# Kernel optimization log

Hardware: AMD Instinct MI355X
Metric: run time of the kernel (lower is better)

Reference implementation:

```python
import jax, jax.numpy as jnp
import numpy as np

B, T, C, H = 2, 2048, 1024, 16
D = C // H  # head dim = 64


def setup_inputs() -> dict:
    key = jax.random.key(0)
    ks = jax.random.split(key, 3)
    x = jax.random.normal(ks[0], (B, T, C), dtype=jnp.float32)
    W_attn = jax.random.normal(ks[1], (C, 3 * C), dtype=jnp.float32) * (1.0 / np.sqrt(C))
    b_attn = jnp.zeros((3 * C,), dtype=jnp.float32)
    W_proj = jax.random.normal(ks[2], (C, C), dtype=jnp.float32) * (1.0 / np.sqrt(C))
    b_proj = jnp.zeros((C,), dtype=jnp.float32)
    return {"x": x, "W_attn": W_attn, "b_attn": b_attn, "W_proj": W_proj, "b_proj": b_proj}


def reference(x, W_attn, b_attn, W_proj, b_proj):
    Bb, Tt, Cc = x.shape
    qkv = x @ W_attn + b_attn                       # [B,T,3C]
    q, k, v = jnp.split(qkv, 3, axis=-1)            # each [B,T,C]
    q = q.reshape(Bb, Tt, H, D).transpose(0, 2, 1, 3)  # [B,H,T,D]
    k = k.reshape(Bb, Tt, H, D).transpose(0, 2, 1, 3)
    v = v.reshape(Bb, Tt, H, D).transpose(0, 2, 1, 3)
    # NOTE: original scales by 1/sqrt(n_embd), not 1/sqrt(head_dim)
    scale = 1.0 / np.sqrt(Cc)
    wei = jnp.einsum('bhqd,bhkd->bhqk', q, k) * scale  # [B,H,T,T]
    causal = jnp.tril(jnp.ones((Tt, Tt), dtype=bool))
    wei = jnp.where(causal, wei, -jnp.inf)
    wei = jax.nn.softmax(wei, axis=-1)
    out = jnp.einsum('bhqk,bhkd->bhqd', wei, v)        # [B,H,T,D]
    out = out.transpose(0, 2, 1, 3).reshape(Bb, Tt, Cc)
    return out @ W_proj + b_proj
```

## Files before the change

### kernel.cpp

```cpp
#include <hip/hip_runtime.h>


typedef short bfrag __attribute__((ext_vector_type(8)));
typedef float facc  __attribute__((ext_vector_type(4)));
typedef float f16v  __attribute__((ext_vector_type(16)));
typedef float f4v   __attribute__((ext_vector_type(4)));
typedef unsigned int u32x2 __attribute__((ext_vector_type(2)));
typedef unsigned int u32x4v __attribute__((ext_vector_type(4)));
typedef unsigned short u16;

#define MFMA16(a, b, c) __builtin_amdgcn_mfma_f32_16x16x32_bf16((a), (b), (c), 0, 0, 0)
#define MFMA32(a, b, c) __builtin_amdgcn_mfma_f32_32x32x16_bf16((a), (b), (c), 0, 0, 0)

__device__ __forceinline__ u16 f2bf(float f) {
  union { float f; unsigned u; } v; v.f = f;
  unsigned r = v.u + 0x7fffu + ((v.u >> 16) & 1u);
  return (u16)(r >> 16);
}

__device__ __forceinline__ unsigned cvtpk(float lo, float hi) {
  unsigned r;
  asm("v_cvt_pk_bf16_f32 %0, %1, %2" : "=v"(r) : "v"(lo), "v"(hi));
  return r;
}

__device__ __forceinline__ void async_lds16(const void* g, void* l) {
  __builtin_amdgcn_global_load_lds(
      (const __attribute__((address_space(1))) unsigned char*)g,
      (__attribute__((address_space(3))) unsigned char*)l, 16, 0, 0);
}


__global__ void cast_bf16_kernel(const float* __restrict__ s, u16* __restrict__ d, int n) {
  int i = (blockIdx.x * blockDim.x + threadIdx.x) * 4;
  if (i >= n) return;
  f4v v = *reinterpret_cast<const f4v*>(s + i);
  u32x2 w;
  w[0] = (unsigned)f2bf(v[0]) | ((unsigned)f2bf(v[1]) << 16);
  w[1] = (unsigned)f2bf(v[2]) | ((unsigned)f2bf(v[3]) << 16);
  *reinterpret_cast<u32x2*>(d + i) = w;
}

__global__ void transpose_cast_kernel(const float* __restrict__ src, u16* __restrict__ dst,
                                      int K, int N) {
  __shared__ float tile[32][33];
  int tx = threadIdx.x, ty = threadIdx.y;
  int n0 = blockIdx.x * 32, k0 = blockIdx.y * 32;
  for (int j = ty; j < 32; j += 8)
    tile[j][tx] = src[(size_t)(k0 + j) * N + (n0 + tx)];
  __syncthreads();
  for (int j = ty; j < 32; j += 8)
    dst[(size_t)(n0 + j) * K + (k0 + tx)] = f2bf(tile[tx][j]);
}


template <int EPI>
__global__ __launch_bounds__(256) void gemm_kernel(
    const u16* __restrict__ A, const u16* __restrict__ Bt,
    const float* __restrict__ bias, float* __restrict__ outf,
    u16* __restrict__ qb, u16* __restrict__ kb, u16* __restrict__ vb) {
  constexpr int KD = 1024;
  __shared__ u16 As[128 * 32];
  __shared__ u16 Bs[128 * 32];
  const int t = threadIdx.x;
  const int l = t & 63, w = t >> 6;
  const int wm = w >> 1, wn = w & 1;
  const int lg = l >> 4, lc = l & 15;
  const int m0 = blockIdx.y * 128, n0 = blockIdx.x * 128;
  facc acc[4][4] = {};
  const int srow = t >> 2, scol = (t & 3) * 8;
  const u16* ga = A + (size_t)(m0 + srow) * KD + scol;
  const u16* gb = Bt + (size_t)(n0 + srow) * KD + scol;
  u16* la0 = As + t * 8;  u16* la1 = As + 2048 + t * 8;
  u16* lb0 = Bs + t * 8;  u16* lb1 = Bs + 2048 + t * 8;
  for (int kt = 0; kt < KD / 32; ++kt) {
    __syncthreads();
    async_lds16(ga + kt * 32, la0);
    async_lds16(ga + 64 * KD + kt * 32, la1);
    async_lds16(gb + kt * 32, lb0);
    async_lds16(gb + 64 * KD + kt * 32, lb1);
    __syncthreads();
    bfrag a[4], b[4];
#pragma unroll
    for (int mi = 0; mi < 4; ++mi)
      a[mi] = *reinterpret_cast<const bfrag*>(As + (wm * 64 + mi * 16 + lc) * 32 + lg * 8);
#pragma unroll
    for (int ni = 0; ni < 4; ++ni)
      b[ni] = *reinterpret_cast<const bfrag*>(Bs + (wn * 64 + ni * 16 + lc) * 32 + lg * 8);
#pragma unroll
    for (int mi = 0; mi < 4; ++mi)
#pragma unroll
      for (int ni = 0; ni < 4; ++ni)
        acc[mi][ni] = MFMA16(a[mi], b[ni], acc[mi][ni]);
  }
#pragma unroll
  for (int mi = 0; mi < 4; ++mi) {
#pragma unroll
    for (int ni = 0; ni < 4; ++ni) {
#pragma unroll
      for (int r = 0; r < 4; ++r) {
        int gm = m0 + wm * 64 + mi * 16 + lg * 4 + r;
        int gn = n0 + wn * 64 + ni * 16 + lc;
        float val = acc[mi][ni][r] + bias[gn];
        if constexpr (EPI == 0) {
          int sec = gn >> 10, ci = gn & 1023;
          int h = ci >> 6, d = ci & 63;
          int b_ = gm >> 11, tq = gm & 2047;
          int bh = b_ * 16 + h;
          if (sec == 0) {
            qb[((size_t)bh * 2048 + tq) * 64 + d] = f2bf(val * 0.045084439f);
          } else if (sec == 1) {
            kb[((size_t)bh * 2048 + tq) * 64 + d] = f2bf(val);
          } else {
            vb[((size_t)bh * 64 + d) * 2048 + tq] = f2bf(val);
          }
        } else {
          outf[(size_t)gm * 1024 + gn] = val;
        }
      }
    }
  }
}


__global__ __launch_bounds__(128, 2) void attn_kernel(
    const u16* __restrict__ Qb, const u16* __restrict__ Kb,
    const u16* __restrict__ Vtb, u16* __restrict__ attn) {
  constexpr int T = 2048;
  __shared__ u16 Ks[2][2][64 * 64];
  const int t = threadIdx.x;
  const int l = t & 63, w = t >> 6;
  const int c = l & 31, h = l >> 5;
  const int b = blockIdx.x;
  const int bh = b & 31;
  const int chunk = 63 - (b >> 5);
  const int ntile = (chunk >> 1) + 1;
  const int nrounds = (ntile + 1) >> 1;
  const int q0 = chunk * 32;
  const size_t base = (size_t)bh * T * 64;
  const u16* Qp = Qb + base;
  const u16* Kp = Kb + base;
  const u16* Vp = Vtb + base;

  bfrag qf[4];
#pragma unroll
  for (int dt = 0; dt < 4; ++dt)
    qf[dt] = *reinterpret_cast<const bfrag*>(Qp + (size_t)(q0 + c) * 64 + dt * 16 + 8 * h);

  f16v o[2] = {};
  f16v s[2];
  float m_ = -1e30f, l_ = 0.f;

  const int srow0 = l >> 3;
  const int sw8   = ((l & 7) ^ (l >> 3)) * 8;
  u16* kb0 = &Ks[0][w][0];
  u16* kb1 = &Ks[1][w][0];

#define STAGE_K(dst, kvb_)                                                       \
  {                                                                              \
    _Pragma("unroll")                                                            \
    for (int j = 0; j < 8; ++j)                                                  \
      async_lds16(Kp + (size_t)((kvb_) + srow0 + 8 * j) * 64 + sw8,              \
                  (dst) + 512 * j);                                              \
  }
#define LOADV(vf, kvb_)                                                          \
  {                                                                              \
    _Pragma("unroll")                                                            \
    for (int nt = 0; nt < 2; ++nt)                                               \
      _Pragma("unroll")                                                          \
      for (int k2 = 0; k2 < 4; ++k2)                                             \
        vf[nt * 4 + k2] = *reinterpret_cast<const bfrag*>(                       \
            Vp + (size_t)(32 * nt + c) * T + (kvb_) + 16 * k2 + 8 * h);          \
  }

  auto qk = [&](const u16* ks) {
    const f16v z = {};
    s[0] = z; s[1] = z;
    __builtin_amdgcn_s_setprio(1);
#pragma unroll
    for (int kt = 0; kt < 2; ++kt)
#pragma unroll
      for (int dt = 0; dt < 4; ++dt) {
        const bfrag a = *reinterpret_cast<const bfrag*>(
            ks + (32 * kt + c) * 64 + (((2 * dt + h) ^ (c & 7)) * 8));
        s[kt] = MFMA32(a, qf[dt], s[kt]);
      }
    __builtin_amdgcn_s_setprio(0);
  };

  auto pv = [&](const bfrag pa[4], const bfrag vf[8]) {
    __builtin_amdgcn_s_setprio(1);
#pragma unroll
    for (int nt = 0; nt < 2; ++nt)
#pragma unroll
      for (int k2 = 0; k2 < 4; ++k2)
        o[nt] = MFMA32(pa[k2], vf[nt * 4 + k2], o[nt]);
    __builtin_amdgcn_s_setprio(0);
  };

  auto softmax_pa = [&](int it, bfrag pa[4]) {
    if (it == ntile - 1) {
      const int kvb = 64 * it;
      const int qq = q0 + c;
#pragma unroll
      for (int kt = 0; kt < 2; ++kt)
#pragma unroll
        for (int r = 0; r < 16; ++r) {
          const int kk = kvb + 32 * kt + (r & 3) + 8 * (r >> 2) + 4 * h;
          if (kk > qq) s[kt][r] = -1e30f;
        }
    }
    float pms[4] = {-1e30f, -1e30f, -1e30f, -1e30f};
#pragma unroll
    for (int kt = 0; kt < 2; ++kt)
#pragma unroll
      for (int r = 0; r < 16; ++r) pms[r & 3] = fmaxf(pms[r & 3], s[kt][r]);
    float pm = fmaxf(fmaxf(pms[0], pms[1]), fmaxf(pms[2], pms[3]));
    pm = fmaxf(pm, __shfl_xor(pm, 32));
    if (!__all(pm <= m_ + 8.0f)) {
      const float mn = fmaxf(m_, pm);
      const float al = exp2f(m_ - mn);
      l_ *= al;
#pragma unroll
      for (int r = 0; r < 16; ++r) {
        const float ar = __shfl(al, (r & 3) + 8 * (r >> 2) + 4 * h);
        o[0][r] *= ar;
        o[1][r] *= ar;
      }
      m_ = mn;
    }
    float ps[4] = {0.f, 0.f, 0.f, 0.f};
#pragma unroll
    for (int kt = 0; kt < 2; ++kt)
#pragma unroll
      for (int r = 0; r < 16; ++r) {
        const float e = exp2f(s[kt][r] - m_);
        s[kt][r] = e;
        ps[r & 3] += e;
      }
    float pss = (ps[0] + ps[1]) + (ps[2] + ps[3]);
    pss += __shfl_xor(pss, 32);
    l_ += pss;
#pragma unroll
    for (int kt = 0; kt < 2; ++kt)
#pragma unroll
      for (int sub = 0; sub < 2; ++sub) {
        const int bs = 8 * sub;
        unsigned x1 = cvtpk(s[kt][bs + 0], s[kt][bs + 1]);
        unsigned y1 = cvtpk(s[kt][bs + 4], s[kt][bs + 5]);
        asm volatile("v_permlane32_swap_b32 %0, %1" : "+v"(x1), "+v"(y1));
        unsigned x2 = cvtpk(s[kt][bs + 2], s[kt][bs + 3]);
        unsigned y2 = cvtpk(s[kt][bs + 6], s[kt][bs + 7]);
        asm volatile("v_permlane32_swap_b32 %0, %1" : "+v"(x2), "+v"(y2));
        union { u32x4v wv; bfrag f; } u;
        u.wv[0] = x1; u.wv[1] = x2; u.wv[2] = y1; u.wv[3] = y2;
        pa[2 * kt + sub] = u.f;
      }
  };

  bfrag vfA[8], vfB[8], pa[4];
  if (w < ntile) { STAGE_K(kb0, 64 * w); LOADV(vfA, 64 * w); }
  __syncthreads();
  for (int r = 0; r < nrounds; ++r) {
    const int it = 2 * r + w;
    const int itn = it + 2;
    if (itn < ntile) {
      if (r & 1) { STAGE_K(kb0, 64 * itn); LOADV(vfA, 64 * itn); }
      else       { STAGE_K(kb1, 64 * itn); LOADV(vfB, 64 * itn); }
    }
    if (it < ntile) {
      qk((r & 1) ? kb1 : kb0);
      softmax_pa(it, pa);
      pv(pa, (r & 1) ? vfB : vfA);
    }
    __syncthreads();
  }

  float* Fo = (float*)&Ks[0][0][0];
  float* Fm = Fo + 64 * 33;
  float* Fl = Fm + 32;
  if (w == 1) {
#pragma unroll
    for (int nt = 0; nt < 2; ++nt)
#pragma unroll
      for (int r = 0; r < 16; ++r) {
        const int row = (r & 3) + 8 * (r >> 2) + 4 * h;
        Fo[(nt * 32 + c) * 33 + row] = o[nt][r];
      }
    if (h == 0) { Fm[c] = m_; Fl[c] = l_; }
  }
  __syncthreads();
  if (w == 0) {
    const float m1v = Fm[c], l1v = Fl[c];
    const float mm = fmaxf(m_, m1v);
    const float a0 = exp2f(m_ - mm), a1 = exp2f(m1v - mm);
    const float linv = 1.0f / (a0 * l_ + a1 * l1v);
    const int b_ = bh >> 4, hd = bh & 15;
#pragma unroll
    for (int r = 0; r < 16; ++r) {
      const int row = (r & 3) + 8 * (r >> 2) + 4 * h;
      const float a0r = __shfl(a0, row);
      const float a1r = __shfl(a1, row);
      const float lr = __shfl(linv, row);
      const int tq = q0 + row;
#pragma unroll
      for (int nt = 0; nt < 2; ++nt) {
        const float o1 = Fo[(nt * 32 + c) * 33 + row];
        attn[((size_t)(b_ * T + tq)) * 1024 + hd * 64 + 32 * nt + c] =
            f2bf((a0r * o[nt][r] + a1r * o1) * lr);
      }
    }
  }
#undef STAGE_K
#undef LOADV
}


extern "C" void kernel_launch(void* const* d_in, const int* in_sizes, int n_in,
                              void* d_out, int out_size, void* d_ws, size_t ws_size,
                              hipStream_t stream) {
  const float* x      = (const float*)d_in[0];
  const float* W_attn = (const float*)d_in[1];
  const float* b_attn = (const float*)d_in[2];
  const float* W_proj = (const float*)d_in[3];
  const float* b_proj = (const float*)d_in[4];
  float* out = (float*)d_out;
  char* ws = (char*)d_ws;
  u16* xb   = (u16*)(ws);
  u16* Wat  = (u16*)(ws + (8u  << 20));
  u16* Wpt  = (u16*)(ws + (14u << 20));
  u16* Qb   = (u16*)(ws + (16u << 20));
  u16* Kb   = (u16*)(ws + (24u << 20));
  u16* Vtb  = (u16*)(ws + (32u << 20));
  u16* attn = (u16*)(ws + (40u << 20));

  cast_bf16_kernel<<<4096, 256, 0, stream>>>(x, xb, 4096 * 1024);
  transpose_cast_kernel<<<dim3(96, 32), dim3(32, 8), 0, stream>>>(W_attn, Wat, 1024, 3072);
  transpose_cast_kernel<<<dim3(32, 32), dim3(32, 8), 0, stream>>>(W_proj, Wpt, 1024, 1024);
  gemm_kernel<0><<<dim3(24, 32), 256, 0, stream>>>(xb, Wat, b_attn, nullptr, Qb, Kb, Vtb);
  attn_kernel<<<2048, 128, 0, stream>>>(Qb, Kb, Vtb, attn);
  gemm_kernel<1><<<dim3(8, 32), 256, 0, stream>>>(attn, Wpt, b_proj, out, nullptr, nullptr, nullptr);
}
```

Measured before the change: 138.8 us.

## Double-buffer GEMM LDS, swizzle GEMM blocks, share K tiles across attention query warps

The GEMM now double-buffers its A/B LDS tiles so the next k-slice loads while the current one computes. It also drops from two barriers to one per k-step and remaps block indices with an 8-way swizzle to improve L2 locality. The attention kernel goes from 128 to 256 threads, so two query sub-blocks of 32 rows share each staged 64-row K tile in LDS, halving K staging per query row and halving the grid. The costs are more LDS per GEMM block and a larger attention block with different occupancy, and the swizzle assumes the grid size is divisible by 8.

```diff
diff --git a/kernel.cpp b/kernel.cpp
--- a/kernel.cpp
+++ b/kernel.cpp
@@ -58,41 +58,51 @@
 __global__ __launch_bounds__(256) void gemm_kernel(
     const u16* __restrict__ A, const u16* __restrict__ Bt,
     const float* __restrict__ bias, float* __restrict__ outf,
-    u16* __restrict__ qb, u16* __restrict__ kb, u16* __restrict__ vb) {
-  constexpr int KD = 1024;
-  __shared__ u16 As[128 * 32];
-  __shared__ u16 Bs[128 * 32];
+    u16* __restrict__ qb, u16* __restrict__ kb, u16* __restrict__ vb, int NX) {
+  constexpr int KD = 1024, NK = KD / 32;
+  __shared__ u16 As[2][128 * 32];
+  __shared__ u16 Bs[2][128 * 32];
   const int t = threadIdx.x;
   const int l = t & 63, w = t >> 6;
   const int wm = w >> 1, wn = w & 1;
   const int lg = l >> 4, lc = l & 15;
-  const int m0 = blockIdx.y * 128, n0 = blockIdx.x * 128;
+  const int nwg = gridDim.x;
+  const int u = blockIdx.x;
+  const int swz = (u & 7) * (nwg >> 3) + (u >> 3);
+  const int m0 = (swz / NX) * 128, n0 = (swz % NX) * 128;
   facc acc[4][4] = {};
   const int srow = t >> 2, scol = (t & 3) * 8;
   const u16* ga = A + (size_t)(m0 + srow) * KD + scol;
   const u16* gb = Bt + (size_t)(n0 + srow) * KD + scol;
-  u16* la0 = As + t * 8;  u16* la1 = As + 2048 + t * 8;
-  u16* lb0 = Bs + t * 8;  u16* lb1 = Bs + 2048 + t * 8;
-  for (int kt = 0; kt < KD / 32; ++kt) {
-    __syncthreads();
-    async_lds16(ga + kt * 32, la0);
-    async_lds16(ga + 64 * KD + kt * 32, la1);
-    async_lds16(gb + kt * 32, lb0);
-    async_lds16(gb + 64 * KD + kt * 32, lb1);
-    __syncthreads();
+
+#define GSTAGE(bi, kt_)                                                          \
+  {                                                                              \
+    async_lds16(ga + (kt_) * 32, As[bi] + t * 8);                                \
+    async_lds16(ga + 64 * KD + (kt_) * 32, As[bi] + 2048 + t * 8);               \
+    async_lds16(gb + (kt_) * 32, Bs[bi] + t * 8);                                \
+    async_lds16(gb + 64 * KD + (kt_) * 32, Bs[bi] + 2048 + t * 8);               \
+  }
+
+  GSTAGE(0, 0);
+  __syncthreads();
+  for (int kt = 0; kt < NK; ++kt) {
+    const int buf = kt & 1;
+    if (kt + 1 < NK) GSTAGE(buf ^ 1, kt + 1);
     bfrag a[4], b[4];
 #pragma unroll
     for (int mi = 0; mi < 4; ++mi)
-      a[mi] = *reinterpret_cast<const bfrag*>(As + (wm * 64 + mi * 16 + lc) * 32 + lg * 8);
+      a[mi] = *reinterpret_cast<const bfrag*>(As[buf] + (wm * 64 + mi * 16 + lc) * 32 + lg * 8);
 #pragma unroll
     for (int ni = 0; ni < 4; ++ni)
-      b[ni] = *reinterpret_cast<const bfrag*>(Bs + (wn * 64 + ni * 16 + lc) * 32 + lg * 8);
+      b[ni] = *reinterpret_cast<const bfrag*>(Bs[buf] + (wn * 64 + ni * 16 + lc) * 32 + lg * 8);
 #pragma unroll
     for (int mi = 0; mi < 4; ++mi)
 #pragma unroll
       for (int ni = 0; ni < 4; ++ni)
         acc[mi][ni] = MFMA16(a[mi], b[ni], acc[mi][ni]);
-  }
+    __syncthreads();
+  }
+#undef GSTAGE
 #pragma unroll
   for (int mi = 0; mi < 4; ++mi) {
 #pragma unroll
@@ -123,20 +133,21 @@
 }
 
 
-__global__ __launch_bounds__(128, 2) void attn_kernel(
+__global__ __launch_bounds__(256, 4) void attn_kernel(
     const u16* __restrict__ Qb, const u16* __restrict__ Kb,
     const u16* __restrict__ Vtb, u16* __restrict__ attn) {
   constexpr int T = 2048;
   __shared__ u16 Ks[2][2][64 * 64];
   const int t = threadIdx.x;
   const int l = t & 63, w = t >> 6;
+  const int wq = w >> 1, ws = w & 1;
   const int c = l & 31, h = l >> 5;
   const int b = blockIdx.x;
   const int bh = b & 31;
-  const int chunk = 63 - (b >> 5);
-  const int ntile = (chunk >> 1) + 1;
+  const int qblk = 31 - (b >> 5);
+  const int ntile = qblk + 1;
   const int nrounds = (ntile + 1) >> 1;
-  const int q0 = chunk * 32;
+  const int q0 = qblk * 64 + wq * 32;
   const size_t base = (size_t)bh * T * 64;
   const u16* Qp = Qb + base;
   const u16* Kp = Kb + base;
@@ -151,17 +162,16 @@
   f16v s[2];
   float m_ = -1e30f, l_ = 0.f;
 
-  const int srow0 = l >> 3;
-  const int sw8   = ((l & 7) ^ (l >> 3)) * 8;
-  u16* kb0 = &Ks[0][w][0];
-  u16* kb1 = &Ks[1][w][0];
-
-#define STAGE_K(dst, kvb_)                                                       \
+  const int srow0 = wq * 8 + (l >> 3);
+  const int sw8   = ((l & 7) ^ ((l >> 3) & 7)) * 8;
+  const int ldso  = wq * 512 + l * 8;
+
+#define STAGE_K(p, tile_)                                                        \
   {                                                                              \
     _Pragma("unroll")                                                            \
-    for (int j = 0; j < 8; ++j)                                                  \
-      async_lds16(Kp + (size_t)((kvb_) + srow0 + 8 * j) * 64 + sw8,              \
-                  (dst) + 512 * j);                                              \
+    for (int j = 0; j < 4; ++j)                                                  \
+      async_lds16(Kp + (size_t)(64 * (tile_) + srow0 + 16 * j) * 64 + sw8,       \
+                  &Ks[p][ws][ldso + 1024 * j]);                                  \
   }
 #define LOADV(vf, kvb_)                                                          \
   {                                                                              \
@@ -259,39 +269,40 @@
   };
 
   bfrag vfA[8], vfB[8], pa[4];
-  if (w < ntile) { STAGE_K(kb0, 64 * w); LOADV(vfA, 64 * w); }
+  if (ws < ntile) { STAGE_K(0, ws); LOADV(vfA, 64 * ws); }
   __syncthreads();
   for (int r = 0; r < nrounds; ++r) {
-    const int it = 2 * r + w;
+    const int p = r & 1;
+    const int it = 2 * r + ws;
     const int itn = it + 2;
     if (itn < ntile) {
-      if (r & 1) { STAGE_K(kb0, 64 * itn); LOADV(vfA, 64 * itn); }
-      else       { STAGE_K(kb1, 64 * itn); LOADV(vfB, 64 * itn); }
+      STAGE_K(p ^ 1, itn);
+      if (p) { LOADV(vfA, 64 * itn); } else { LOADV(vfB, 64 * itn); }
     }
     if (it < ntile) {
-      qk((r & 1) ? kb1 : kb0);
+      qk(&Ks[p][ws][0]);
       softmax_pa(it, pa);
-      pv(pa, (r & 1) ? vfB : vfA);
+      pv(pa, p ? vfB : vfA);
     }
     __syncthreads();
   }
 
   float* Fo = (float*)&Ks[0][0][0];
-  float* Fm = Fo + 64 * 33;
-  float* Fl = Fm + 32;
-  if (w == 1) {
+  float* Fm = Fo + 2 * 64 * 33;
+  float* Fl = Fm + 64;
+  if (ws == 1) {
 #pragma unroll
     for (int nt = 0; nt < 2; ++nt)
 #pragma unroll
       for (int r = 0; r < 16; ++r) {
         const int row = (r & 3) + 8 * (r >> 2) + 4 * h;
-        Fo[(nt * 32 + c) * 33 + row] = o[nt][r];
-      }
-    if (h == 0) { Fm[c] = m_; Fl[c] = l_; }
+        Fo[(wq * 64 + nt * 32 + c) * 33 + row] = o[nt][r];
+      }
+    if (h == 0) { Fm[wq * 32 + c] = m_; Fl[wq * 32 + c] = l_; }
   }
   __syncthreads();
-  if (w == 0) {
-    const float m1v = Fm[c], l1v = Fl[c];
+  if (ws == 0) {
+    const float m1v = Fm[wq * 32 + c], l1v = Fl[wq * 32 + c];
     const float mm = fmaxf(m_, m1v);
     const float a0 = exp2f(m_ - mm), a1 = exp2f(m1v - mm);
     const float linv = 1.0f / (a0 * l_ + a1 * l1v);
@@ -305,7 +316,7 @@
       const int tq = q0 + row;
 #pragma unroll
       for (int nt = 0; nt < 2; ++nt) {
-        const float o1 = Fo[(nt * 32 + c) * 33 + row];
+        const float o1 = Fo[(wq * 64 + nt * 32 + c) * 33 + row];
         attn[((size_t)(b_ * T + tq)) * 1024 + hd * 64 + 32 * nt + c] =
             f2bf((a0r * o[nt][r] + a1r * o1) * lr);
       }
@@ -337,7 +348,7 @@
   cast_bf16_kernel<<<4096, 256, 0, stream>>>(x, xb, 4096 * 1024);
   transpose_cast_kernel<<<dim3(96, 32), dim3(32, 8), 0, stream>>>(W_attn, Wat, 1024, 3072);
   transpose_cast_kernel<<<dim3(32, 32), dim3(32, 8), 0, stream>>>(W_proj, Wpt, 1024, 1024);
-  gemm_kernel<0><<<dim3(24, 32), 256, 0, stream>>>(xb, Wat, b_attn, nullptr, Qb, Kb, Vtb);
-  attn_kernel<<<2048, 128, 0, stream>>>(Qb, Kb, Vtb, attn);
-  gemm_kernel<1><<<dim3(8, 32), 256, 0, stream>>>(attn, Wpt, b_proj, out, nullptr, nullptr, nullptr);
-}
+  gemm_kernel<0><<<768, 256, 0, stream>>>(xb, Wat, b_attn, nullptr, Qb, Kb, Vtb, 24);
+  attn_kernel<<<1024, 256, 0, stream>>>(Qb, Kb, Vtb, attn);
+  gemm_kernel<1><<<256, 256, 0, stream>>>(attn, Wpt, b_proj, out, nullptr, nullptr, nullptr, 8);
+}
```

Result: slower. 303.8 us (+118.9%).
